# Optimization experiments

Hardware: AMD Instinct MI355X
Metric: run time of the kernel (lower is better)

The kernel has to match this reference:

```python
import jax, jax.numpy as jnp
import numpy as np

B, H, W = 32, 512, 512
LAM = 1.0


def _pdist(x):
    # x: (n, d) -> (n, n) euclidean distance matrix (torch.cdist equivalent)
    sq = jnp.sum(x * x, axis=-1)
    d2 = sq[:, None] + sq[None, :] - 2.0 * (x @ x.T)
    return jnp.sqrt(jnp.maximum(d2, 0.0))


def _mst_edges(D):
    # 0-dim Vietoris-Rips persistence pairing == edges of the minimum spanning
    # tree of the distance matrix. Prim's algorithm, n-1 sequential steps.
    n = D.shape[0]
    big = jnp.asarray(jnp.finfo(D.dtype).max, D.dtype)
    in_tree = jnp.zeros(n, dtype=bool).at[0].set(True)
    min_dist = D[0].at[0].set(big)          # best distance from tree to each node
    min_from = jnp.zeros(n, dtype=jnp.int32)  # tree endpoint achieving min_dist

    def step(carry, _):
        in_tree, md, mf = carry
        j = jnp.argmin(jnp.where(in_tree, big, md)).astype(jnp.int32)
        i = mf[j]
        in_tree = in_tree.at[j].set(True)
        better = (D[j] < md) & (~in_tree)
        md = jnp.where(better, D[j], md)
        mf = jnp.where(better, j, mf)
        return (in_tree, md, mf), (i, j)

    _, (us, vs) = jax.lax.scan(step, (in_tree, min_dist, min_from), None, length=n - 1)
    return us, vs  # each (n-1,) int32


def _topo_loss_single(x, z):
    # x, z: (n, d) point clouds (prediction / mask rows as points)
    Dx = _pdist(x)
    Dz = _pdist(z)
    # SignatureLoss normalisation: divide distance matrices by their max
    Dx = Dx / jnp.maximum(Dx.max(), 1e-12)
    Dz = Dz / jnp.maximum(Dz.max(), 1e-12)
    # persistence pairings (dim 0) of each space
    ux, vx = _mst_edges(jax.lax.stop_gradient(Dx))
    uz, vz = _mst_edges(jax.lax.stop_gradient(Dz))
    # signature loss (Topological Autoencoders, p=2):
    # ||D_X[pi_X] - D_Z[pi_X]||_2^2 + ||D_X[pi_Z] - D_Z[pi_Z]||_2^2
    t1 = jnp.sum((Dx[ux, vx] - Dz[ux, vx]) ** 2)
    t2 = jnp.sum((Dx[uz, vz] - Dz[uz, vz]) ** 2)
    return t1 + t2


def setup_inputs() -> dict:
    key = jax.random.key(0)
    k1, k2 = jax.random.split(key)
    model_output = jax.random.normal(k1, (B, 1, H, W), dtype=jnp.float32)
    labels = jax.random.uniform(k2, (B, 1, H, W), dtype=jnp.float32)
    return {"model_output": model_output, "labels": labels}


def reference(model_output, labels):
    preds = jax.nn.sigmoid(jnp.squeeze(model_output, axis=1))  # (B, H, W)
    masks = jnp.squeeze(labels, axis=1)                        # (B, H, W)
    losses = jax.vmap(_topo_loss_single)(preds, masks)         # (B,)
    return LAM * jnp.sum(losses) / preds.shape[0]
```

## Files before the change

### kernel.cpp

```cpp
#include <hip/hip_runtime.h>
#include <math.h>

#define NN 512
#define NN2 (NN*NN)
#define NB 32
#define NM 64

typedef __attribute__((ext_vector_type(8))) short short8v;
typedef __attribute__((ext_vector_type(4))) float f32x4;

typedef const unsigned int __attribute__((address_space(1)))* gas_ptr;
typedef unsigned int __attribute__((address_space(3)))* las_ptr;

__device__ __forceinline__ float sigm(float x) { return 1.0f / (1.0f + expf(-x)); }

__device__ __forceinline__ unsigned short f2bf(float x) {
  unsigned u = __float_as_uint(x);
  return (unsigned short)((u + 0x7fffu + ((u >> 16) & 1u)) >> 16);
}
__device__ __forceinline__ float bf2f(unsigned short h) {
  return __uint_as_float(((unsigned)h) << 16);
}
__device__ __forceinline__ unsigned long long u64min(unsigned long long a,
                                                     unsigned long long b) {
  return (b < a) ? b : a;
}
__device__ __forceinline__ void amin64(unsigned long long* p, unsigned long long v) {
  unsigned long long old = *p;
  while (v < old) {
    unsigned long long assumed = old;
    old = atomicCAS(p, assumed, v);
    if (old == assumed) break;
  }
}
template <int CTRL>
__device__ __forceinline__ unsigned long long dpp_min_u64(unsigned long long x) {
  int xlo = (int)(unsigned)x, xhi = (int)(unsigned)(x >> 32);
  int ylo = __builtin_amdgcn_update_dpp(xlo, xlo, CTRL, 0xf, 0xf, false);
  int yhi = __builtin_amdgcn_update_dpp(xhi, xhi, CTRL, 0xf, 0xf, false);
  unsigned long long y = ((unsigned long long)(unsigned)yhi << 32) | (unsigned)ylo;
  return (y < x) ? y : x;
}
__device__ __forceinline__ unsigned long long wave_min_u64(unsigned long long k) {
  k = dpp_min_u64<0x111>(k); k = dpp_min_u64<0x112>(k);
  k = dpp_min_u64<0x114>(k); k = dpp_min_u64<0x118>(k);
  k = dpp_min_u64<0x142>(k); k = dpp_min_u64<0x143>(k);
  return k;
}
__device__ __forceinline__ unsigned long long grp16_min_u64(unsigned long long k) {
  k = dpp_min_u64<0x111>(k); k = dpp_min_u64<0x112>(k);
  k = dpp_min_u64<0x114>(k); k = dpp_min_u64<0x118>(k);
  return k;
}

__global__ __launch_bounds__(256) void split_kernel(const float* __restrict__ model,
                                                    const float* __restrict__ labels,
                                                    unsigned short* __restrict__ Hi,
                                                    unsigned short* __restrict__ Lo,
                                                    float* __restrict__ sq, int m0) {
  int b = blockIdx.x;
  int mL = b >> 8;
  int m = m0 + mL;
  int tid = threadIdx.x;
  size_t off = (size_t)(b & 255) * 1024 + tid * 4;
  const float* src = ((m & 1) ? labels + (size_t)(m >> 1) * NN2
                              : model + (size_t)(m >> 1) * NN2) + off;
  float4 v = *(const float4*)src;
  if (!(m & 1)) { v.x = sigm(v.x); v.y = sigm(v.y); v.z = sigm(v.z); v.w = sigm(v.w); }
  ushort4 h, l;
  h.x = f2bf(v.x); l.x = f2bf(v.x - bf2f(h.x));
  h.y = f2bf(v.y); l.y = f2bf(v.y - bf2f(h.y));
  h.z = f2bf(v.z); l.z = f2bf(v.z - bf2f(h.z));
  h.w = f2bf(v.w); l.w = f2bf(v.w - bf2f(h.w));
  *(ushort4*)(Hi + (size_t)mL * NN2 + off) = h;
  *(ushort4*)(Lo + (size_t)mL * NN2 + off) = l;
  float s = v.x * v.x + v.y * v.y + v.z * v.z + v.w * v.w;
  #pragma unroll
  for (int o = 32; o > 0; o >>= 1) s += __shfl_down(s, o);
  __shared__ float red[4];
  if ((tid & 63) == 0) red[tid >> 6] = s;
  __syncthreads();
  if (tid == 0) {
    int row0 = (b & 255) * 2;
    sq[(size_t)m * NN + row0]     = red[0] + red[1];
    sq[(size_t)m * NN + row0 + 1] = red[2] + red[3];
  }
}

__global__ __launch_bounds__(256, 3) void gemm_dist(const unsigned short* __restrict__ Hi,
                                                    const unsigned short* __restrict__ Lo,
                                                    const float* __restrict__ sq,
                                                    float* __restrict__ Dreg,
                                                    unsigned* __restrict__ maxBits,
                                                    unsigned long long* __restrict__ best1,
                                                    int m0, int nm) {
  __shared__ unsigned short P[4][128 * 32];
  int id = blockIdx.x;
  int p, mL;
  if ((nm & 7) == 0) {
    int x = id & 7, t = id >> 3;
    p = t % 10;
    mL = x + 8 * (t / 10);
  } else {
    p = id % 10;
    mL = id / 10;
  }
  int by = (p >= 4) + (p >= 7) + (p >= 9);
  int bx = p - ((by * (7 - by)) >> 1);
  bool diag = (by == bx);
  int m = m0 + mL;
  const unsigned short* Hm = Hi + (size_t)mL * NN2;
  const unsigned short* Lm = Lo + (size_t)mL * NN2;

  int tid = threadIdx.x;
  int wid = tid >> 6, lane = tid & 63;
  int wy = wid >> 1, wx = wid & 1;
  int lr = lane & 15, lk = lane >> 4;

  const unsigned short* wsrcM = (wid & 1) ? Lm : Hm;
  int wrow0 = (wid < 2) ? by * 128 : bx * 128;
  bool stage = (!diag) || (wid < 2);
  int srow = lane >> 2;
  int schunk = (lane & 3) ^ ((lane >> 3) & 3);
  const unsigned short* gsrc = wsrcM + (size_t)(wrow0 + srow) * NN + schunk * 8;
  unsigned short* ldst = &P[wid & 3][0];

  f32x4 acc[4][4];
  #pragma unroll
  for (int i = 0; i < 4; ++i)
    #pragma unroll
    for (int j = 0; j < 4; ++j) acc[i][j] = (f32x4){0.f, 0.f, 0.f, 0.f};

  const unsigned short* bAh = &P[0][0];
  const unsigned short* bAl = &P[1][0];
  const unsigned short* bBh = diag ? &P[0][0] : &P[2][0];
  const unsigned short* bBl = diag ? &P[1][0] : &P[3][0];
  int sw = (lr >> 1) & 3;
  int rao = (wy * 64 + lr) * 32 + (lk ^ sw) * 8;
  int rbo = (wx * 64 + lr) * 32 + (lk ^ sw) * 8;

  for (int s = 0; s < 16; ++s) {
    int k0 = s * 32;
    if (stage) {
      #pragma unroll
      for (int i = 0; i < 8; ++i)
        __builtin_amdgcn_global_load_lds(
            (gas_ptr)(const void*)(gsrc + k0 + (size_t)i * 16 * NN),
            (las_ptr)(void*)(ldst + i * 512), 16, 0, 0);
    }
    __syncthreads();

    short8v fa[4], fb[4], fb2[4];
    #pragma unroll
    for (int i = 0; i < 4; ++i) {
      fa[i] = *(const short8v*)(bAh + rao + i * 16 * 32);
      fb[i] = *(const short8v*)(bBh + rbo + i * 16 * 32);
    }
    #pragma unroll
    for (int mi = 0; mi < 4; ++mi)
      #pragma unroll
      for (int ni = 0; ni < 4; ++ni)
        acc[mi][ni] = __builtin_amdgcn_mfma_f32_16x16x32_bf16(fa[mi], fb[ni], acc[mi][ni], 0, 0, 0);
    #pragma unroll
    for (int i = 0; i < 4; ++i)
      fb2[i] = *(const short8v*)(bBl + rbo + i * 16 * 32);
    #pragma unroll
    for (int mi = 0; mi < 4; ++mi)
      #pragma unroll
      for (int ni = 0; ni < 4; ++ni)
        acc[mi][ni] = __builtin_amdgcn_mfma_f32_16x16x32_bf16(fa[mi], fb2[ni], acc[mi][ni], 0, 0, 0);
    #pragma unroll
    for (int i = 0; i < 4; ++i)
      fa[i] = *(const short8v*)(bAl + rao + i * 16 * 32);
    #pragma unroll
    for (int mi = 0; mi < 4; ++mi)
      #pragma unroll
      for (int ni = 0; ni < 4; ++ni)
        acc[mi][ni] = __builtin_amdgcn_mfma_f32_16x16x32_bf16(fa[mi], fb[ni], acc[mi][ni], 0, 0, 0);
    __syncthreads();
  }

  const float* sqm = sq + (size_t)m * NN;
  float* Dm = Dreg + (size_t)mL * NN2;
  int gr0 = by * 128 + wy * 64;
  int gc0 = bx * 128 + wx * 64;
  float tmax = 0.f;
  unsigned long long* b1 = best1 + (size_t)m * NN;
  unsigned long long ck[4];
  #pragma unroll
  for (int i = 0; i < 4; ++i) ck[i] = ~0ull;

  #pragma unroll
  for (int mi = 0; mi < 4; ++mi) {
    int rb = gr0 + mi * 16 + lk * 4;
    float sqi0 = sqm[rb + 0], sqi1 = sqm[rb + 1], sqi2 = sqm[rb + 2], sqi3 = sqm[rb + 3];
    unsigned long long rk[4];
    #pragma unroll
    for (int j = 0; j < 4; ++j) rk[j] = ~0ull;
    #pragma unroll
    for (int ni = 0; ni < 4; ++ni) {
      int col = gc0 + ni * 16 + lr;
      float sqj = sqm[col];
      f32x4 a = acc[mi][ni];
      float v0 = sqrtf(fmaxf(sqi0 + sqj - 2.f * a[0], 0.f));
      float v1 = sqrtf(fmaxf(sqi1 + sqj - 2.f * a[1], 0.f));
      float v2 = sqrtf(fmaxf(sqi2 + sqj - 2.f * a[2], 0.f));
      float v3 = sqrtf(fmaxf(sqi3 + sqj - 2.f * a[3], 0.f));
      Dm[(size_t)(rb + 0) * NN + col] = v0;
      Dm[(size_t)(rb + 1) * NN + col] = v1;
      Dm[(size_t)(rb + 2) * NN + col] = v2;
      Dm[(size_t)(rb + 3) * NN + col] = v3;
      if (!diag)
        *(float4*)(Dm + (size_t)col * NN + rb) = make_float4(v0, v1, v2, v3);
      tmax = fmaxf(tmax, fmaxf(fmaxf(v0, v1), fmaxf(v2, v3)));
      float vv[4] = {v0, v1, v2, v3};
      #pragma unroll
      for (int rg = 0; rg < 4; ++rg) {
        int row = rb + rg;
        if (!diag || col != row) {
          unsigned lo = (row < col) ? (unsigned)(row * NN + col)
                                    : (unsigned)(col * NN + row);
          unsigned long long key =
              ((unsigned long long)__float_as_uint(vv[rg]) << 32) | lo;
          rk[rg] = u64min(rk[rg], key);
          ck[ni] = u64min(ck[ni], key);
        }
      }
    }
    #pragma unroll
    for (int rg = 0; rg < 4; ++rg) {
      unsigned long long k = grp16_min_u64(rk[rg]);
      if (lr == 15) atomicMin(&b1[rb + rg], k);
    }
  }
  if (!diag) {
    #pragma unroll
    for (int ni = 0; ni < 4; ++ni) {
      unsigned long long k = ck[ni];
      k = u64min(k, __shfl_xor(k, 16));
      k = u64min(k, __shfl_xor(k, 32));
      if (lk == 0) atomicMin(&b1[gc0 + ni * 16 + lr], k);
    }
  }
  #pragma unroll
  for (int off = 32; off > 0; off >>= 1) tmax = fmaxf(tmax, __shfl_down(tmax, off));
  if (lane == 0) atomicMax(&maxBits[m], __float_as_uint(tmax));
}

__global__ __launch_bounds__(512) void hook1_kernel(const unsigned long long* __restrict__ best1,
                                                    int* __restrict__ compG,
                                                    int2* __restrict__ eo_all,
                                                    int* __restrict__ ecntG, int m0) {
  int mL = blockIdx.x, m = m0 + mL;
  const unsigned long long* b1 = best1 + (size_t)m * NN;
  int2* eo = eo_all + (size_t)m * (NN - 1);
  __shared__ int hook[NN], parent[NN];
  __shared__ int ecnt;
  int tid = threadIdx.x;
  if (tid == 0) ecnt = 0;
  unsigned long long b = b1[tid];
  int h;
  if (b != ~0ull) {
    int idx = (int)(unsigned)b;
    int er = idx >> 9, ec = idx & 511;
    h = (er == tid) ? ec : er;
  } else h = tid;
  hook[tid] = h;
  __syncthreads();
  bool active = (b != ~0ull);
  int p = h;
  bool mutual = active && (hook[p] == tid);
  parent[tid] = (!active) ? tid : ((mutual && tid < p) ? tid : p);
  if (active && (!mutual || tid > p)) {
    int idx = (int)(unsigned)b;
    int e = atomicAdd(&ecnt, 1);
    eo[e] = make_int2(idx >> 9, idx & 511);
  }
  __syncthreads();
  int c = tid, pp = parent[c];
  while (pp != c) { c = pp; pp = parent[c]; }
  compG[(size_t)m * NN + tid] = c;
  if (tid == 0) ecntG[m] = ecnt;
}

__global__ __launch_bounds__(512) void scan2_kernel(const float* __restrict__ Dreg,
                                                    const int* __restrict__ compG,
                                                    unsigned long long* __restrict__ best2,
                                                    int m0) {
  int sblk = blockIdx.x, mL = blockIdx.y, m = m0 + mL;
  const float* D = Dreg + (size_t)mL * NN2;
  __shared__ int compP[NN + 64];
  int tid = threadIdx.x;
  int wave = tid >> 6, lane = tid & 63;
  int c0 = lane * 8;
  if (tid < NN) compP[tid + (tid >> 3)] = compG[(size_t)m * NN + tid];
  __syncthreads();
  unsigned long long* b2 = best2 + (size_t)m * NN;
  #pragma unroll
  for (int rr = 0; rr < 8; ++rr) {
    int r = sblk * 64 + wave * 8 + rr;
    int cr = compP[r + (r >> 3)];
    const float4* rp = (const float4*)(D + (size_t)r * NN + c0);
    float4 v0 = rp[0], v1 = rp[1];
    int4 cc0 = *(const int4*)(compP + c0 + (c0 >> 3));
    int4 cc1 = *(const int4*)(compP + c0 + 4 + (c0 >> 3));
    float vv[8] = {v0.x, v0.y, v0.z, v0.w, v1.x, v1.y, v1.z, v1.w};
    int cv[8] = {cc0.x, cc0.y, cc0.z, cc0.w, cc1.x, cc1.y, cc1.z, cc1.w};
    unsigned long long k = ~0ull;
    #pragma unroll
    for (int e = 0; e < 8; ++e) {
      if (cv[e] != cr) {
        int col = c0 + e;
        int lo = (r < col) ? r * NN + col : col * NN + r;
        unsigned long long key = ((unsigned long long)__float_as_uint(vv[e]) << 32) | (unsigned)lo;
        k = u64min(k, key);
      }
    }
    k = wave_min_u64(k);
    if (lane == 63 && k != ~0ull) atomicMin(&b2[cr], k);
  }
}

__global__ __launch_bounds__(512) void hook2_kernel(const unsigned long long* __restrict__ best2,
                                                    const int* __restrict__ compG,
                                                    int* __restrict__ comp2g,
                                                    int2* __restrict__ eo_all,
                                                    int* __restrict__ ecntG,
                                                    int* __restrict__ cntG, int m0) {
  int mL = blockIdx.x, m = m0 + mL;
  const unsigned long long* b2 = best2 + (size_t)m * NN;
  int2* eo = eo_all + (size_t)m * (NN - 1);
  __shared__ int comp[NN], hook[NN], parent[NN], dmap[NN];
  __shared__ int ecnt, ccnt;
  int tid = threadIdx.x;
  if (tid == 0) { ecnt = ecntG[m]; ccnt = 0; }
  comp[tid] = compG[(size_t)m * NN + tid];
  __syncthreads();
  unsigned long long b = b2[tid];
  int h;
  if (b != ~0ull) {
    int idx = (int)(unsigned)b;
    int er = idx >> 9, ec = idx & 511;
    int c1 = comp[er], c2 = comp[ec];
    h = (c1 == tid) ? c2 : c1;
  } else h = tid;
  hook[tid] = h;
  __syncthreads();
  bool active = (b != ~0ull);
  int p = h;
  bool mutual = active && (hook[p] == tid);
  parent[tid] = (!active) ? tid : ((mutual && tid < p) ? tid : p);
  if (active && (!mutual || tid > p)) {
    int idx = (int)(unsigned)b;
    int e = atomicAdd(&ecnt, 1);
    eo[e] = make_int2(idx >> 9, idx & 511);
  }
  __syncthreads();
  int c = comp[tid], pp = parent[c];
  while (pp != c) { c = pp; pp = parent[c]; }
  __syncthreads();
  comp[tid] = c;
  __syncthreads();
  if (comp[tid] == tid) dmap[tid] = atomicAdd(&ccnt, 1);
  __syncthreads();
  comp2g[(size_t)m * NN + tid] = dmap[comp[tid]];
  if (tid == 0) { ecntG[m] = ecnt; cntG[m] = ccnt; }
}

__global__ __launch_bounds__(512) void contract_kernel(const float* __restrict__ Dreg,
                                                       const int* __restrict__ comp2g,
                                                       unsigned long long* __restrict__ DcG,
                                                       int m0) {
  int q = blockIdx.x, mL = blockIdx.y, m = m0 + mL;
  const float* D = Dreg + (size_t)mL * NN2;
  __shared__ unsigned long long Dc[128 * 128];
  __shared__ int c2P[NN + 64];
  int tid = threadIdx.x;
  int wave = tid >> 6, lane = tid & 63;
  int c0 = lane * 8;
  if (tid < NN) c2P[tid + (tid >> 3)] = comp2g[(size_t)m * NN + tid];
  for (int i = tid; i < 16384; i += 512) Dc[i] = ~0ull;
  __syncthreads();
  #pragma unroll
  for (int rr = 0; rr < 16; ++rr) {
    int r = q * 128 + wave * 16 + rr;
    int di = c2P[r + (r >> 3)];
    const float4* rp = (const float4*)(D + (size_t)r * NN + c0);
    float4 v0 = rp[0], v1 = rp[1];
    int4 cc0 = *(const int4*)(c2P + c0 + (c0 >> 3));
    int4 cc1 = *(const int4*)(c2P + c0 + 4 + (c0 >> 3));
    float vv[8] = {v0.x, v0.y, v0.z, v0.w, v1.x, v1.y, v1.z, v1.w};
    int cv[8] = {cc0.x, cc0.y, cc0.z, cc0.w, cc1.x, cc1.y, cc1.z, cc1.w};
    #pragma unroll
    for (int e = 0; e < 8; ++e) {
      if (cv[e] != di) {
        int col = c0 + e;
        int lo = (r < col) ? r * NN + col : col * NN + r;
        unsigned long long key = ((unsigned long long)__float_as_uint(vv[e]) << 32) | (unsigned)lo;
        amin64(&Dc[di * 128 + cv[e]], key);
      }
    }
  }
  __syncthreads();
  unsigned long long* dg = DcG + (size_t)mL * 16384;
  for (int i = tid; i < 16384; i += 512) {
    unsigned long long v = Dc[i];
    if (v != ~0ull) atomicMin(&dg[i], v);
  }
}

__global__ __launch_bounds__(1024) void finish_kernel(const float* __restrict__ Dreg,
                                                      const unsigned long long* __restrict__ DcG,
                                                      const int* __restrict__ comp2g,
                                                      const int* __restrict__ cntG,
                                                      int2* __restrict__ eo_all,
                                                      int* __restrict__ ecntG,
                                                      const unsigned* __restrict__ maxBits,
                                                      float* __restrict__ out, int m0) {
  int mL = blockIdx.x, m = m0 + mL;
  __shared__ unsigned long long Dc[16384];
  __shared__ int c2n[NN];
  __shared__ unsigned long long best[128];
  __shared__ int comp2[128], hook128[128], parent128[128];
  __shared__ float fred[16];
  __shared__ int ecnt;
  int tid = threadIdx.x;
  int wave = tid >> 6, lane = tid & 63;
  const unsigned long long* dg = DcG + (size_t)mL * 16384;
  for (int i = tid; i < 16384; i += 1024) Dc[i] = dg[i];
  if (tid < NN) c2n[tid] = comp2g[(size_t)m * NN + tid];
  if (tid < 128) comp2[tid] = tid;
  if (tid == 0) ecnt = ecntG[m];
  __syncthreads();
  int C = cntG[m];
  int2* eo = eo_all + (size_t)m * (NN - 1);

  for (int ph = 0; ph < 7; ++ph) {
    if (ecnt >= NN - 1) break;
    if (tid < 128) best[tid] = ~0ull;
    __syncthreads();
    for (int i = tid; i < C * 128; i += 1024) {
      unsigned long long key = Dc[i];
      if (key == ~0ull) continue;
      int a = i >> 7, bb = i & 127;
      int ca = comp2[a], cb = comp2[bb];
      if (ca != cb) amin64(&best[ca], key);
    }
    __syncthreads();
    if (tid < C) {
      unsigned long long b = best[tid];
      int h;
      if (b != ~0ull) {
        int pid = (int)(unsigned)b;
        int er = pid >> 9, ec = pid & 511;
        int c1 = comp2[c2n[er]], c2v = comp2[c2n[ec]];
        h = (c1 == tid) ? c2v : c1;
      } else h = tid;
      hook128[tid] = h;
    }
    __syncthreads();
    if (tid < C) {
      unsigned long long b = best[tid];
      bool active = (b != ~0ull);
      int p = hook128[tid];
      bool mutual = active && (hook128[p] == tid);
      parent128[tid] = (!active) ? tid : ((mutual && tid < p) ? tid : p);
      if (active && (!mutual || tid > p)) {
        int pid = (int)(unsigned)b;
        int e = atomicAdd(&ecnt, 1);
        eo[e] = make_int2(pid >> 9, pid & 511);
      }
    }
    __syncthreads();
    if (tid < C) {
      int c = comp2[tid], pp = parent128[c];
      while (pp != c) { c = pp; pp = parent128[c]; }
      comp2[tid] = c;
    }
    __syncthreads();
  }
  __syncthreads();

  int b = m >> 1;
  float mxX = fmaxf(__uint_as_float(maxBits[2 * b]), 1e-12f);
  float mxZ = fmaxf(__uint_as_float(maxBits[2 * b + 1]), 1e-12f);
  float rX = 1.0f / mxX, rZ = 1.0f / mxZ;
  const float* Dx = Dreg + (size_t)(mL & ~1) * NN2;
  const float* Dz = Dx + NN2;
  float acc = 0.f;
  if (tid < NN - 1) {
    int2 e = eo[tid];
    size_t off = (size_t)e.x * NN + e.y;
    float d = Dx[off] * rX - Dz[off] * rZ;
    acc = d * d;
  }
  #pragma unroll
  for (int o = 32; o > 0; o >>= 1) acc += __shfl_down(acc, o);
  if (lane == 0) fred[wave] = acc;
  __syncthreads();
  if (tid == 0) {
    float t = 0.f;
    #pragma unroll
    for (int i = 0; i < 16; ++i) t += fred[i];
    atomicAdd(out, t * (1.0f / NB));
  }
}

extern "C" void kernel_launch(void* const* d_in, const int* in_sizes, int n_in,
                              void* d_out, int out_size, void* d_ws, size_t ws_size,
                              hipStream_t stream) {
  const float* model = (const float*)d_in[0];
  const float* labels = (const float*)d_in[1];
  float* out = (float*)d_out;
  char* ws = (char*)d_ws;

  float*              sq      = (float*)(ws);
  unsigned*           maxBits = (unsigned*)(ws + 131072);
  int2*               eo      = (int2*)(ws + 132096);
  unsigned long long* best1   = (unsigned long long*)(ws + 393728);
  unsigned long long* best2   = (unsigned long long*)(ws + 655872);
  int*                compG   = (int*)(ws + 918016);
  int*                comp2g  = (int*)(ws + 1049088);
  int*                ecntG   = (int*)(ws + 1180160);
  int*                cntG    = (int*)(ws + 1180416);
  size_t base = 1181696;

  size_t perBatch = 2ull * (NN2 * sizeof(float) + 2ull * NN2 * 2 + 16384 * 8);
  size_t dcap = (ws_size > base) ? (ws_size - base) : 0;
  int cb = (int)(dcap / perBatch);
  if (cb > NB) cb = NB;
  if (cb < 1) cb = 1;
  int nmc = 2 * cb;

  float* Dreg = (float*)(ws + base);
  unsigned short* Hi = (unsigned short*)(ws + base + (size_t)nmc * NN2 * sizeof(float));
  unsigned short* Lo = Hi + (size_t)nmc * NN2;
  unsigned long long* DcG = (unsigned long long*)(Lo + (size_t)nmc * NN2);

  hipMemsetAsync(d_out, 0, sizeof(float), stream);
  hipMemsetAsync(maxBits, 0, 64 * sizeof(unsigned), stream);

  for (int b0 = 0; b0 < NB; b0 += cb) {
    int nb = (NB - b0 < cb) ? (NB - b0) : cb;
    int nm = 2 * nb, m0 = 2 * b0;
    hipMemsetAsync(best1 + (size_t)m0 * NN, 0xFF, (size_t)nm * NN * 16, stream);
    hipMemsetAsync(DcG, 0xFF, (size_t)nm * 16384 * 8, stream);
    split_kernel<<<nm * 256, 256, 0, stream>>>(model, labels, Hi, Lo, sq, m0);
    gemm_dist<<<10 * nm, 256, 0, stream>>>(Hi, Lo, sq, Dreg, maxBits, best1, m0, nm);
    hook1_kernel<<<nm, 512, 0, stream>>>(best1, compG, eo, ecntG, m0);
    scan2_kernel<<<dim3(8, nm), 512, 0, stream>>>(Dreg, compG, best2, m0);
    hook2_kernel<<<nm, 512, 0, stream>>>(best2, compG, comp2g, eo, ecntG, cntG, m0);
    contract_kernel<<<dim3(4, nm), 512, 0, stream>>>(Dreg, comp2g, DcG, m0);
    finish_kernel<<<nm, 1024, 0, stream>>>(Dreg, DcG, comp2g, cntG, eo, ecntG,
                                           maxBits, out, m0);
  }
}
```

Baseline: 149.2 us.

## Skip second Boruvka round; contract graph after first hook pass

After: 187.3 us. +25.5%, slower.

```diff
diff --git a/kernel.cpp b/kernel.cpp
--- a/kernel.cpp
+++ b/kernel.cpp
@@ -40,12 +40,6 @@
   int yhi = __builtin_amdgcn_update_dpp(xhi, xhi, CTRL, 0xf, 0xf, false);
   unsigned long long y = ((unsigned long long)(unsigned)yhi << 32) | (unsigned)ylo;
   return (y < x) ? y : x;
-}
-__device__ __forceinline__ unsigned long long wave_min_u64(unsigned long long k) {
-  k = dpp_min_u64<0x111>(k); k = dpp_min_u64<0x112>(k);
-  k = dpp_min_u64<0x114>(k); k = dpp_min_u64<0x118>(k);
-  k = dpp_min_u64<0x142>(k); k = dpp_min_u64<0x143>(k);
-  return k;
 }
 __device__ __forceinline__ unsigned long long grp16_min_u64(unsigned long long k) {
   k = dpp_min_u64<0x111>(k); k = dpp_min_u64<0x112>(k);
@@ -249,15 +243,16 @@
 
 __global__ __launch_bounds__(512) void hook1_kernel(const unsigned long long* __restrict__ best1,
                                                     int* __restrict__ compG,
+                                                    int* __restrict__ cntG,
                                                     int2* __restrict__ eo_all,
                                                     int* __restrict__ ecntG, int m0) {
   int mL = blockIdx.x, m = m0 + mL;
   const unsigned long long* b1 = best1 + (size_t)m * NN;
   int2* eo = eo_all + (size_t)m * (NN - 1);
-  __shared__ int hook[NN], parent[NN];
-  __shared__ int ecnt;
+  __shared__ int hook[NN], parent[NN], dmap[NN];
+  __shared__ int ecnt, ccnt;
   int tid = threadIdx.x;
-  if (tid == 0) ecnt = 0;
+  if (tid == 0) { ecnt = 0; ccnt = 0; }
   unsigned long long b = b1[tid];
   int h;
   if (b != ~0ull) {
@@ -279,171 +274,91 @@
   __syncthreads();
   int c = tid, pp = parent[c];
   while (pp != c) { c = pp; pp = parent[c]; }
-  compG[(size_t)m * NN + tid] = c;
-  if (tid == 0) ecntG[m] = ecnt;
-}
-
-__global__ __launch_bounds__(512) void scan2_kernel(const float* __restrict__ Dreg,
-                                                    const int* __restrict__ compG,
-                                                    unsigned long long* __restrict__ best2,
-                                                    int m0) {
-  int sblk = blockIdx.x, mL = blockIdx.y, m = m0 + mL;
+  if (parent[tid] == tid) dmap[tid] = atomicAdd(&ccnt, 1);
+  __syncthreads();
+  compG[(size_t)m * NN + tid] = dmap[c];
+  if (tid == 0) { ecntG[m] = ecnt; cntG[m] = ccnt; }
+}
+
+__global__ __launch_bounds__(512) void scan2c_kernel(const float* __restrict__ Dreg,
+                                                     const int* __restrict__ compG,
+                                                     unsigned long long* __restrict__ DcG,
+                                                     int m0) {
+  int q = blockIdx.x, mL = blockIdx.y, m = m0 + mL;
   const float* D = Dreg + (size_t)mL * NN2;
+  __shared__ unsigned long long Dp[64 * 256];
   __shared__ int compP[NN + 64];
+  __shared__ int rowc[64];
   int tid = threadIdx.x;
   int wave = tid >> 6, lane = tid & 63;
   int c0 = lane * 8;
   if (tid < NN) compP[tid + (tid >> 3)] = compG[(size_t)m * NN + tid];
-  __syncthreads();
-  unsigned long long* b2 = best2 + (size_t)m * NN;
+  for (int i = tid; i < 16384; i += 512) Dp[i] = ~0ull;
+  __syncthreads();
   #pragma unroll
   for (int rr = 0; rr < 8; ++rr) {
-    int r = sblk * 64 + wave * 8 + rr;
-    int cr = compP[r + (r >> 3)];
+    int rslot = wave * 8 + rr;
+    int r = q * 64 + rslot;
+    int da = compP[r + (r >> 3)];
+    if (lane == 0) rowc[rslot] = da;
     const float4* rp = (const float4*)(D + (size_t)r * NN + c0);
     float4 v0 = rp[0], v1 = rp[1];
     int4 cc0 = *(const int4*)(compP + c0 + (c0 >> 3));
     int4 cc1 = *(const int4*)(compP + c0 + 4 + (c0 >> 3));
     float vv[8] = {v0.x, v0.y, v0.z, v0.w, v1.x, v1.y, v1.z, v1.w};
     int cv[8] = {cc0.x, cc0.y, cc0.z, cc0.w, cc1.x, cc1.y, cc1.z, cc1.w};
-    unsigned long long k = ~0ull;
     #pragma unroll
     for (int e = 0; e < 8; ++e) {
-      if (cv[e] != cr) {
+      if (cv[e] != da) {
         int col = c0 + e;
         int lo = (r < col) ? r * NN + col : col * NN + r;
         unsigned long long key = ((unsigned long long)__float_as_uint(vv[e]) << 32) | (unsigned)lo;
-        k = u64min(k, key);
+        amin64(&Dp[rslot * 256 + cv[e]], key);
       }
     }
-    k = wave_min_u64(k);
-    if (lane == 63 && k != ~0ull) atomicMin(&b2[cr], k);
-  }
-}
-
-__global__ __launch_bounds__(512) void hook2_kernel(const unsigned long long* __restrict__ best2,
-                                                    const int* __restrict__ compG,
-                                                    int* __restrict__ comp2g,
-                                                    int2* __restrict__ eo_all,
-                                                    int* __restrict__ ecntG,
-                                                    int* __restrict__ cntG, int m0) {
+  }
+  __syncthreads();
+  unsigned long long* dg = DcG + (size_t)mL * 65536;
+  for (int i = tid; i < 16384; i += 512) {
+    unsigned long long v = Dp[i];
+    if (v != ~0ull) atomicMin(&dg[(size_t)rowc[i >> 8] * 256 + (i & 255)], v);
+  }
+}
+
+__global__ __launch_bounds__(1024) void finishAll_kernel(const float* __restrict__ Dreg,
+                                                         const unsigned long long* __restrict__ DcG,
+                                                         const int* __restrict__ compG,
+                                                         const int* __restrict__ cntG,
+                                                         int2* __restrict__ eo_all,
+                                                         int* __restrict__ ecntG,
+                                                         const unsigned* __restrict__ maxBits,
+                                                         float* __restrict__ out, int m0) {
   int mL = blockIdx.x, m = m0 + mL;
-  const unsigned long long* b2 = best2 + (size_t)m * NN;
-  int2* eo = eo_all + (size_t)m * (NN - 1);
-  __shared__ int comp[NN], hook[NN], parent[NN], dmap[NN];
-  __shared__ int ecnt, ccnt;
-  int tid = threadIdx.x;
-  if (tid == 0) { ecnt = ecntG[m]; ccnt = 0; }
-  comp[tid] = compG[(size_t)m * NN + tid];
-  __syncthreads();
-  unsigned long long b = b2[tid];
-  int h;
-  if (b != ~0ull) {
-    int idx = (int)(unsigned)b;
-    int er = idx >> 9, ec = idx & 511;
-    int c1 = comp[er], c2 = comp[ec];
-    h = (c1 == tid) ? c2 : c1;
-  } else h = tid;
-  hook[tid] = h;
-  __syncthreads();
-  bool active = (b != ~0ull);
-  int p = h;
-  bool mutual = active && (hook[p] == tid);
-  parent[tid] = (!active) ? tid : ((mutual && tid < p) ? tid : p);
-  if (active && (!mutual || tid > p)) {
-    int idx = (int)(unsigned)b;
-    int e = atomicAdd(&ecnt, 1);
-    eo[e] = make_int2(idx >> 9, idx & 511);
-  }
-  __syncthreads();
-  int c = comp[tid], pp = parent[c];
-  while (pp != c) { c = pp; pp = parent[c]; }
-  __syncthreads();
-  comp[tid] = c;
-  __syncthreads();
-  if (comp[tid] == tid) dmap[tid] = atomicAdd(&ccnt, 1);
-  __syncthreads();
-  comp2g[(size_t)m * NN + tid] = dmap[comp[tid]];
-  if (tid == 0) { ecntG[m] = ecnt; cntG[m] = ccnt; }
-}
-
-__global__ __launch_bounds__(512) void contract_kernel(const float* __restrict__ Dreg,
-                                                       const int* __restrict__ comp2g,
-                                                       unsigned long long* __restrict__ DcG,
-                                                       int m0) {
-  int q = blockIdx.x, mL = blockIdx.y, m = m0 + mL;
-  const float* D = Dreg + (size_t)mL * NN2;
-  __shared__ unsigned long long Dc[128 * 128];
-  __shared__ int c2P[NN + 64];
-  int tid = threadIdx.x;
-  int wave = tid >> 6, lane = tid & 63;
-  int c0 = lane * 8;
-  if (tid < NN) c2P[tid + (tid >> 3)] = comp2g[(size_t)m * NN + tid];
-  for (int i = tid; i < 16384; i += 512) Dc[i] = ~0ull;
-  __syncthreads();
-  #pragma unroll
-  for (int rr = 0; rr < 16; ++rr) {
-    int r = q * 128 + wave * 16 + rr;
-    int di = c2P[r + (r >> 3)];
-    const float4* rp = (const float4*)(D + (size_t)r * NN + c0);
-    float4 v0 = rp[0], v1 = rp[1];
-    int4 cc0 = *(const int4*)(c2P + c0 + (c0 >> 3));
-    int4 cc1 = *(const int4*)(c2P + c0 + 4 + (c0 >> 3));
-    float vv[8] = {v0.x, v0.y, v0.z, v0.w, v1.x, v1.y, v1.z, v1.w};
-    int cv[8] = {cc0.x, cc0.y, cc0.z, cc0.w, cc1.x, cc1.y, cc1.z, cc1.w};
-    #pragma unroll
-    for (int e = 0; e < 8; ++e) {
-      if (cv[e] != di) {
-        int col = c0 + e;
-        int lo = (r < col) ? r * NN + col : col * NN + r;
-        unsigned long long key = ((unsigned long long)__float_as_uint(vv[e]) << 32) | (unsigned)lo;
-        amin64(&Dc[di * 128 + cv[e]], key);
-      }
-    }
-  }
-  __syncthreads();
-  unsigned long long* dg = DcG + (size_t)mL * 16384;
-  for (int i = tid; i < 16384; i += 512) {
-    unsigned long long v = Dc[i];
-    if (v != ~0ull) atomicMin(&dg[i], v);
-  }
-}
-
-__global__ __launch_bounds__(1024) void finish_kernel(const float* __restrict__ Dreg,
-                                                      const unsigned long long* __restrict__ DcG,
-                                                      const int* __restrict__ comp2g,
-                                                      const int* __restrict__ cntG,
-                                                      int2* __restrict__ eo_all,
-                                                      int* __restrict__ ecntG,
-                                                      const unsigned* __restrict__ maxBits,
-                                                      float* __restrict__ out, int m0) {
-  int mL = blockIdx.x, m = m0 + mL;
-  __shared__ unsigned long long Dc[16384];
-  __shared__ int c2n[NN];
-  __shared__ unsigned long long best[128];
-  __shared__ int comp2[128], hook128[128], parent128[128];
+  __shared__ int c1n[NN];
+  __shared__ unsigned long long best[256];
+  __shared__ int compD[256], hookD[256], parentD[256];
   __shared__ float fred[16];
   __shared__ int ecnt;
   int tid = threadIdx.x;
   int wave = tid >> 6, lane = tid & 63;
-  const unsigned long long* dg = DcG + (size_t)mL * 16384;
-  for (int i = tid; i < 16384; i += 1024) Dc[i] = dg[i];
-  if (tid < NN) c2n[tid] = comp2g[(size_t)m * NN + tid];
-  if (tid < 128) comp2[tid] = tid;
+  const unsigned long long* dg = DcG + (size_t)mL * 65536;
+  if (tid < NN) c1n[tid] = compG[(size_t)m * NN + tid];
+  if (tid < 256) compD[tid] = tid;
   if (tid == 0) ecnt = ecntG[m];
   __syncthreads();
   int C = cntG[m];
+  int total = C * 256;
   int2* eo = eo_all + (size_t)m * (NN - 1);
 
-  for (int ph = 0; ph < 7; ++ph) {
+  for (int ph = 0; ph < 8; ++ph) {
     if (ecnt >= NN - 1) break;
-    if (tid < 128) best[tid] = ~0ull;
-    __syncthreads();
-    for (int i = tid; i < C * 128; i += 1024) {
-      unsigned long long key = Dc[i];
+    if (tid < 256) best[tid] = ~0ull;
+    __syncthreads();
+    for (int i = tid; i < total; i += 1024) {
+      unsigned long long key = dg[i];
       if (key == ~0ull) continue;
-      int a = i >> 7, bb = i & 127;
-      int ca = comp2[a], cb = comp2[bb];
+      int a = i >> 8, bb = i & 255;
+      int ca = compD[a], cb = compD[bb];
       if (ca != cb) amin64(&best[ca], key);
     }
     __syncthreads();
@@ -453,18 +368,18 @@
       if (b != ~0ull) {
         int pid = (int)(unsigned)b;
         int er = pid >> 9, ec = pid & 511;
-        int c1 = comp2[c2n[er]], c2v = comp2[c2n[ec]];
+        int c1 = compD[c1n[er]], c2v = compD[c1n[ec]];
         h = (c1 == tid) ? c2v : c1;
       } else h = tid;
-      hook128[tid] = h;
+      hookD[tid] = h;
     }
     __syncthreads();
     if (tid < C) {
       unsigned long long b = best[tid];
       bool active = (b != ~0ull);
-      int p = hook128[tid];
-      bool mutual = active && (hook128[p] == tid);
-      parent128[tid] = (!active) ? tid : ((mutual && tid < p) ? tid : p);
+      int p = hookD[tid];
+      bool mutual = active && (hookD[p] == tid);
+      parentD[tid] = (!active) ? tid : ((mutual && tid < p) ? tid : p);
       if (active && (!mutual || tid > p)) {
         int pid = (int)(unsigned)b;
         int e = atomicAdd(&ecnt, 1);
@@ -473,9 +388,9 @@
     }
     __syncthreads();
     if (tid < C) {
-      int c = comp2[tid], pp = parent128[c];
-      while (pp != c) { c = pp; pp = parent128[c]; }
-      comp2[tid] = c;
+      int c = compD[tid], pp = parentD[c];
+      while (pp != c) { c = pp; pp = parentD[c]; }
+      compD[tid] = c;
     }
     __syncthreads();
   }
@@ -518,14 +433,12 @@
   unsigned*           maxBits = (unsigned*)(ws + 131072);
   int2*               eo      = (int2*)(ws + 132096);
   unsigned long long* best1   = (unsigned long long*)(ws + 393728);
-  unsigned long long* best2   = (unsigned long long*)(ws + 655872);
-  int*                compG   = (int*)(ws + 918016);
-  int*                comp2g  = (int*)(ws + 1049088);
-  int*                ecntG   = (int*)(ws + 1180160);
-  int*                cntG    = (int*)(ws + 1180416);
-  size_t base = 1181696;
-
-  size_t perBatch = 2ull * (NN2 * sizeof(float) + 2ull * NN2 * 2 + 16384 * 8);
+  int*                compG   = (int*)(ws + 655872);
+  int*                ecntG   = (int*)(ws + 786944);
+  int*                cntG    = (int*)(ws + 787200);
+  size_t base = 787456;
+
+  size_t perBatch = 2ull * (NN2 * sizeof(float) + 2ull * NN2 * 2 + 65536ull * 8);
   size_t dcap = (ws_size > base) ? (ws_size - base) : 0;
   int cb = (int)(dcap / perBatch);
   if (cb > NB) cb = NB;
@@ -543,15 +456,13 @@
   for (int b0 = 0; b0 < NB; b0 += cb) {
     int nb = (NB - b0 < cb) ? (NB - b0) : cb;
     int nm = 2 * nb, m0 = 2 * b0;
-    hipMemsetAsync(best1 + (size_t)m0 * NN, 0xFF, (size_t)nm * NN * 16, stream);
-    hipMemsetAsync(DcG, 0xFF, (size_t)nm * 16384 * 8, stream);
+    hipMemsetAsync(best1 + (size_t)m0 * NN, 0xFF, (size_t)nm * NN * 8, stream);
+    hipMemsetAsync(DcG, 0xFF, (size_t)nm * 65536 * 8, stream);
     split_kernel<<<nm * 256, 256, 0, stream>>>(model, labels, Hi, Lo, sq, m0);
     gemm_dist<<<10 * nm, 256, 0, stream>>>(Hi, Lo, sq, Dreg, maxBits, best1, m0, nm);
-    hook1_kernel<<<nm, 512, 0, stream>>>(best1, compG, eo, ecntG, m0);
-    scan2_kernel<<<dim3(8, nm), 512, 0, stream>>>(Dreg, compG, best2, m0);
-    hook2_kernel<<<nm, 512, 0, stream>>>(best2, compG, comp2g, eo, ecntG, cntG, m0);
-    contract_kernel<<<dim3(4, nm), 512, 0, stream>>>(Dreg, comp2g, DcG, m0);
-    finish_kernel<<<nm, 1024, 0, stream>>>(Dreg, DcG, comp2g, cntG, eo, ecntG,
-                                           maxBits, out, m0);
-  }
-}
+    hook1_kernel<<<nm, 512, 0, stream>>>(best1, compG, cntG, eo, ecntG, m0);
+    scan2c_kernel<<<dim3(8, nm), 512, 0, stream>>>(Dreg, compG, DcG, m0);
+    finishAll_kernel<<<nm, 1024, 0, stream>>>(Dreg, DcG, compG, cntG, eo, ecntG,
+                                              maxBits, out, m0);
+  }
+}
```

## Double-buffer LDS tiles in gemm_dist and use DPP for wave min

Applied to the files above, without the earlier changes.

Result: slower. 154.8 us (+3.8%).

```diff
diff --git a/kernel.cpp b/kernel.cpp
--- a/kernel.cpp
+++ b/kernel.cpp
@@ -94,7 +94,7 @@
                                                     unsigned* __restrict__ maxBits,
                                                     unsigned long long* __restrict__ best1,
                                                     int m0, int nm) {
-  __shared__ unsigned short P[4][128 * 32];
+  __shared__ unsigned short P[2][4][4096];
   int id = blockIdx.x;
   int p, mL;
   if ((nm & 7) == 0) {
@@ -119,11 +119,11 @@
 
   const unsigned short* wsrcM = (wid & 1) ? Lm : Hm;
   int wrow0 = (wid < 2) ? by * 128 : bx * 128;
-  bool stage = (!diag) || (wid < 2);
+  bool stg = (!diag) || (wid < 2);
   int srow = lane >> 2;
   int schunk = (lane & 3) ^ ((lane >> 3) & 3);
   const unsigned short* gsrc = wsrcM + (size_t)(wrow0 + srow) * NN + schunk * 8;
-  unsigned short* ldst = &P[wid & 3][0];
+  unsigned short* ldst0 = &P[0][wid & 3][0];
 
   f32x4 acc[4][4];
   #pragma unroll
@@ -131,30 +131,40 @@
     #pragma unroll
     for (int j = 0; j < 4; ++j) acc[i][j] = (f32x4){0.f, 0.f, 0.f, 0.f};
 
-  const unsigned short* bAh = &P[0][0];
-  const unsigned short* bAl = &P[1][0];
-  const unsigned short* bBh = diag ? &P[0][0] : &P[2][0];
-  const unsigned short* bBl = diag ? &P[1][0] : &P[3][0];
+  const unsigned short* base0 = &P[0][0][0];
+  int offAh = 0, offAl = 4096;
+  int offBh = diag ? 0 : 8192, offBl = diag ? 4096 : 12288;
   int sw = (lr >> 1) & 3;
   int rao = (wy * 64 + lr) * 32 + (lk ^ sw) * 8;
   int rbo = (wx * 64 + lr) * 32 + (lk ^ sw) * 8;
 
+  if (stg) {
+    #pragma unroll
+    for (int i = 0; i < 8; ++i)
+      __builtin_amdgcn_global_load_lds(
+          (gas_ptr)(const void*)(gsrc + (size_t)i * 16 * NN),
+          (las_ptr)(void*)(ldst0 + i * 512), 16, 0, 0);
+  }
+
+  int cur = 0;
   for (int s = 0; s < 16; ++s) {
-    int k0 = s * 32;
-    if (stage) {
+    __syncthreads();
+    if (s < 15 && stg) {
+      int k0 = (s + 1) * 32;
+      unsigned short* ld = ldst0 + (cur ^ 1) * 16384;
       #pragma unroll
       for (int i = 0; i < 8; ++i)
         __builtin_amdgcn_global_load_lds(
             (gas_ptr)(const void*)(gsrc + k0 + (size_t)i * 16 * NN),
-            (las_ptr)(void*)(ldst + i * 512), 16, 0, 0);
-    }
-    __syncthreads();
+            (las_ptr)(void*)(ld + i * 512), 16, 0, 0);
+    }
+    const unsigned short* bb = base0 + cur * 16384;
 
     short8v fa[4], fb[4], fb2[4];
     #pragma unroll
     for (int i = 0; i < 4; ++i) {
-      fa[i] = *(const short8v*)(bAh + rao + i * 16 * 32);
-      fb[i] = *(const short8v*)(bBh + rbo + i * 16 * 32);
+      fa[i] = *(const short8v*)(bb + offAh + rao + i * 512);
+      fb[i] = *(const short8v*)(bb + offBh + rbo + i * 512);
     }
     #pragma unroll
     for (int mi = 0; mi < 4; ++mi)
@@ -163,7 +173,7 @@
         acc[mi][ni] = __builtin_amdgcn_mfma_f32_16x16x32_bf16(fa[mi], fb[ni], acc[mi][ni], 0, 0, 0);
     #pragma unroll
     for (int i = 0; i < 4; ++i)
-      fb2[i] = *(const short8v*)(bBl + rbo + i * 16 * 32);
+      fb2[i] = *(const short8v*)(bb + offBl + rbo + i * 512);
     #pragma unroll
     for (int mi = 0; mi < 4; ++mi)
       #pragma unroll
@@ -171,13 +181,13 @@
         acc[mi][ni] = __builtin_amdgcn_mfma_f32_16x16x32_bf16(fa[mi], fb2[ni], acc[mi][ni], 0, 0, 0);
     #pragma unroll
     for (int i = 0; i < 4; ++i)
-      fa[i] = *(const short8v*)(bAl + rao + i * 16 * 32);
+      fa[i] = *(const short8v*)(bb + offAl + rao + i * 512);
     #pragma unroll
     for (int mi = 0; mi < 4; ++mi)
       #pragma unroll
       for (int ni = 0; ni < 4; ++ni)
         acc[mi][ni] = __builtin_amdgcn_mfma_f32_16x16x32_bf16(fa[mi], fb[ni], acc[mi][ni], 0, 0, 0);
-    __syncthreads();
+    cur ^= 1;
   }
 
   const float* sqm = sq + (size_t)m * NN;
@@ -316,7 +326,9 @@
         k = u64min(k, key);
       }
     }
-    k = wave_min_u64(k);
+    k = dpp_min_u64<0x111>(k); k = dpp_min_u64<0x112>(k);
+    k = dpp_min_u64<0x114>(k); k = dpp_min_u64<0x118>(k);
+    k = dpp_min_u64<0x142>(k); k = dpp_min_u64<0x143>(k);
     if (lane == 63 && k != ~0ull) atomicMin(&b2[cr], k);
   }
 }
```

## Stage distance-tile stores through LDS and fuse hook1 into scan2

Applied to the files above, without the earlier changes.

After: 144.8 us. -2.9%, faster.

```diff
diff --git a/kernel.cpp b/kernel.cpp
--- a/kernel.cpp
+++ b/kernel.cpp
@@ -94,7 +94,7 @@
                                                     unsigned* __restrict__ maxBits,
                                                     unsigned long long* __restrict__ best1,
                                                     int m0, int nm) {
-  __shared__ unsigned short P[4][128 * 32];
+  __shared__ unsigned short P[4][4096];
   int id = blockIdx.x;
   int p, mL;
   if ((nm & 7) == 0) {
@@ -153,8 +153,8 @@
     short8v fa[4], fb[4], fb2[4];
     #pragma unroll
     for (int i = 0; i < 4; ++i) {
-      fa[i] = *(const short8v*)(bAh + rao + i * 16 * 32);
-      fb[i] = *(const short8v*)(bBh + rbo + i * 16 * 32);
+      fa[i] = *(const short8v*)(bAh + rao + i * 512);
+      fb[i] = *(const short8v*)(bBh + rbo + i * 512);
     }
     #pragma unroll
     for (int mi = 0; mi < 4; ++mi)
@@ -163,7 +163,7 @@
         acc[mi][ni] = __builtin_amdgcn_mfma_f32_16x16x32_bf16(fa[mi], fb[ni], acc[mi][ni], 0, 0, 0);
     #pragma unroll
     for (int i = 0; i < 4; ++i)
-      fb2[i] = *(const short8v*)(bBl + rbo + i * 16 * 32);
+      fb2[i] = *(const short8v*)(bBl + rbo + i * 512);
     #pragma unroll
     for (int mi = 0; mi < 4; ++mi)
       #pragma unroll
@@ -171,7 +171,7 @@
         acc[mi][ni] = __builtin_amdgcn_mfma_f32_16x16x32_bf16(fa[mi], fb2[ni], acc[mi][ni], 0, 0, 0);
     #pragma unroll
     for (int i = 0; i < 4; ++i)
-      fa[i] = *(const short8v*)(bAl + rao + i * 16 * 32);
+      fa[i] = *(const short8v*)(bAl + rao + i * 512);
     #pragma unroll
     for (int mi = 0; mi < 4; ++mi)
       #pragma unroll
@@ -206,12 +206,8 @@
       float v1 = sqrtf(fmaxf(sqi1 + sqj - 2.f * a[1], 0.f));
       float v2 = sqrtf(fmaxf(sqi2 + sqj - 2.f * a[2], 0.f));
       float v3 = sqrtf(fmaxf(sqi3 + sqj - 2.f * a[3], 0.f));
-      Dm[(size_t)(rb + 0) * NN + col] = v0;
-      Dm[(size_t)(rb + 1) * NN + col] = v1;
-      Dm[(size_t)(rb + 2) * NN + col] = v2;
-      Dm[(size_t)(rb + 3) * NN + col] = v3;
-      if (!diag)
-        *(float4*)(Dm + (size_t)col * NN + rb) = make_float4(v0, v1, v2, v3);
+      acc[mi][ni][0] = v0; acc[mi][ni][1] = v1;
+      acc[mi][ni][2] = v2; acc[mi][ni][3] = v3;
       tmax = fmaxf(tmax, fmaxf(fmaxf(v0, v1), fmaxf(v2, v3)));
       float vv[4] = {v0, v1, v2, v3};
       #pragma unroll
@@ -242,23 +238,68 @@
       if (lk == 0) atomicMin(&b1[gc0 + ni * 16 + lr], k);
     }
   }
+
+  __syncthreads();
+  float* W = (float*)&P[0][0] + wid * 1088;
+  int rlo = lane >> 4, cq = lane & 15;
+  #pragma unroll
+  for (int mi = 0; mi < 4; ++mi) {
+    #pragma unroll
+    for (int ni = 0; ni < 4; ++ni)
+      #pragma unroll
+      for (int j = 0; j < 4; ++j)
+        W[(lk * 4 + j) * 68 + ni * 16 + lr] = acc[mi][ni][j];
+    #pragma unroll
+    for (int g = 0; g < 4; ++g) {
+      int r16 = g * 4 + rlo;
+      float4 t = *(const float4*)&W[r16 * 68 + cq * 4];
+      *(float4*)(Dm + (size_t)(gr0 + mi * 16 + r16) * NN + gc0 + cq * 4) = t;
+    }
+  }
+  if (!diag) {
+    #pragma unroll
+    for (int ni = 0; ni < 4; ++ni) {
+      #pragma unroll
+      for (int mi = 0; mi < 4; ++mi) {
+        f32x4 a = acc[mi][ni];
+        *(float4*)&W[lr * 68 + mi * 16 + lk * 4] = make_float4(a[0], a[1], a[2], a[3]);
+      }
+      #pragma unroll
+      for (int g = 0; g < 4; ++g) {
+        int r16 = g * 4 + rlo;
+        float4 t = *(const float4*)&W[r16 * 68 + cq * 4];
+        *(float4*)(Dm + (size_t)(gc0 + ni * 16 + r16) * NN + gr0 + cq * 4) = t;
+      }
+    }
+  }
+
   #pragma unroll
   for (int off = 32; off > 0; off >>= 1) tmax = fmaxf(tmax, __shfl_down(tmax, off));
   if (lane == 0) atomicMax(&maxBits[m], __float_as_uint(tmax));
 }
 
-__global__ __launch_bounds__(512) void hook1_kernel(const unsigned long long* __restrict__ best1,
+__global__ __launch_bounds__(512) void scan2_kernel(const float* __restrict__ Dreg,
+                                                    const unsigned long long* __restrict__ best1,
                                                     int* __restrict__ compG,
+                                                    unsigned long long* __restrict__ best2,
+                                                    unsigned long long* __restrict__ DcG,
                                                     int2* __restrict__ eo_all,
                                                     int* __restrict__ ecntG, int m0) {
-  int mL = blockIdx.x, m = m0 + mL;
-  const unsigned long long* b1 = best1 + (size_t)m * NN;
-  int2* eo = eo_all + (size_t)m * (NN - 1);
+  int sblk = blockIdx.x, mL = blockIdx.y, m = m0 + mL;
+  const float* D = Dreg + (size_t)mL * NN2;
+  __shared__ int compP[NN + 64];
   __shared__ int hook[NN], parent[NN];
   __shared__ int ecnt;
   int tid = threadIdx.x;
+  int wave = tid >> 6, lane = tid & 63;
+  int c0 = lane * 8;
+
+  unsigned long long* dginit = DcG + (size_t)mL * 16384 + sblk * 2048;
+  #pragma unroll
+  for (int i = 0; i < 4; ++i) dginit[tid + i * 512] = ~0ull;
+
   if (tid == 0) ecnt = 0;
-  unsigned long long b = b1[tid];
+  unsigned long long b = best1[(size_t)m * NN + tid];
   int h;
   if (b != ~0ull) {
     int idx = (int)(unsigned)b;
@@ -271,30 +312,21 @@
   int p = h;
   bool mutual = active && (hook[p] == tid);
   parent[tid] = (!active) ? tid : ((mutual && tid < p) ? tid : p);
-  if (active && (!mutual || tid > p)) {
+  if (sblk == 0 && active && (!mutual || tid > p)) {
     int idx = (int)(unsigned)b;
     int e = atomicAdd(&ecnt, 1);
-    eo[e] = make_int2(idx >> 9, idx & 511);
+    eo_all[(size_t)m * (NN - 1) + e] = make_int2(idx >> 9, idx & 511);
   }
   __syncthreads();
   int c = tid, pp = parent[c];
   while (pp != c) { c = pp; pp = parent[c]; }
-  compG[(size_t)m * NN + tid] = c;
-  if (tid == 0) ecntG[m] = ecnt;
-}
-
-__global__ __launch_bounds__(512) void scan2_kernel(const float* __restrict__ Dreg,
-                                                    const int* __restrict__ compG,
-                                                    unsigned long long* __restrict__ best2,
-                                                    int m0) {
-  int sblk = blockIdx.x, mL = blockIdx.y, m = m0 + mL;
-  const float* D = Dreg + (size_t)mL * NN2;
-  __shared__ int compP[NN + 64];
-  int tid = threadIdx.x;
-  int wave = tid >> 6, lane = tid & 63;
-  int c0 = lane * 8;
-  if (tid < NN) compP[tid + (tid >> 3)] = compG[(size_t)m * NN + tid];
-  __syncthreads();
+  compP[tid + (tid >> 3)] = c;
+  if (sblk == 0) {
+    compG[(size_t)m * NN + tid] = c;
+    if (tid == 0) ecntG[m] = ecnt;
+  }
+  __syncthreads();
+
   unsigned long long* b2 = best2 + (size_t)m * NN;
   #pragma unroll
   for (int rr = 0; rr < 8; ++rr) {
@@ -544,11 +576,10 @@
     int nb = (NB - b0 < cb) ? (NB - b0) : cb;
     int nm = 2 * nb, m0 = 2 * b0;
     hipMemsetAsync(best1 + (size_t)m0 * NN, 0xFF, (size_t)nm * NN * 16, stream);
-    hipMemsetAsync(DcG, 0xFF, (size_t)nm * 16384 * 8, stream);
     split_kernel<<<nm * 256, 256, 0, stream>>>(model, labels, Hi, Lo, sq, m0);
     gemm_dist<<<10 * nm, 256, 0, stream>>>(Hi, Lo, sq, Dreg, maxBits, best1, m0, nm);
-    hook1_kernel<<<nm, 512, 0, stream>>>(best1, compG, eo, ecntG, m0);
-    scan2_kernel<<<dim3(8, nm), 512, 0, stream>>>(Dreg, compG, best2, m0);
+    scan2_kernel<<<dim3(8, nm), 512, 0, stream>>>(Dreg, best1, compG, best2, DcG,
+                                                  eo, ecntG, m0);
     hook2_kernel<<<nm, 512, 0, stream>>>(best2, compG, comp2g, eo, ecntG, cntG, m0);
     contract_kernel<<<dim3(4, nm), 512, 0, stream>>>(Dreg, comp2g, DcG, m0);
     finish_kernel<<<nm, 1024, 0, stream>>>(Dreg, DcG, comp2g, cntG, eo, ecntG,
```
